# Performance work log

Hardware: AMD Instinct MI355X
Metric: run time of the kernel (lower is better)

The kernel has to match this reference:

```python
import jax, jax.numpy as jnp
import numpy as np

IN_F = 4096
OUT_F = 4096
GROUP = 128                      # quantization group size
NG = IN_F * OUT_F // GROUP       # 131072 groups
LORA_R = 16
LORA_SCALE = 32.0 / 16.0         # lora_alpha / lora_r


def _dequant(indices, codebook, scales):
    # Unpack two INT4 nibbles per byte: low nibble first, then high (interleaved).
    low = indices & 15
    high = (indices >> 4) & 15
    idx = jnp.stack([low, high], axis=1).reshape(-1)          # [numel]
    # Codebook lookup, per-group scaling.
    vals = codebook[idx].reshape(NG, GROUP) * scales[:, None]  # [NG, GROUP]
    return vals.reshape(OUT_F, IN_F)


def setup_inputs() -> dict:
    key = jax.random.key(0)
    ks = jax.random.split(key, 7)
    return {
        "x": jax.random.normal(ks[0], (4, 2048, IN_F), dtype=jnp.float32),
        "indices": jax.random.randint(ks[1], (IN_F * OUT_F // 2,), 0, 256, dtype=jnp.int32),
        "codebook": jax.random.normal(ks[2], (16,), dtype=jnp.float32),
        "scales": jax.random.uniform(ks[3], (NG,), dtype=jnp.float32, minval=0.01, maxval=1.0),
        "lora_A": jax.random.normal(ks[4], (IN_F, LORA_R), dtype=jnp.float32) / 64.0,
        "lora_B": jax.random.normal(ks[5], (LORA_R, OUT_F), dtype=jnp.float32) / 64.0,
        "bias": jax.random.normal(ks[6], (OUT_F,), dtype=jnp.float32),
    }


def reference(x, indices, codebook, scales, lora_A, lora_B, bias):
    # lowram path: dequantize INT4 codebook weights, F.linear, fused LoRA add, bias.
    W = _dequant(indices, codebook, scales)                    # [OUT_F, IN_F]
    h = jnp.einsum('bsi,oi->bso', x, W)                        # F.linear (no bias yet)
    h = h + (x @ lora_A) @ lora_B * LORA_SCALE                 # LoRA adapter (dropout=0)
    return h + bias
```

## Files before the change

kernel.cpp:

```cpp
#include <hip/hip_runtime.h>
#include <stdint.h>

#define IN_F   4096
#define OUT_F  4096
#define M_TOT  8192
#define KDIM   4096

typedef float          f32x4  __attribute__((ext_vector_type(4)));
typedef int            i32x4  __attribute__((ext_vector_type(4)));
typedef unsigned short u16x8  __attribute__((ext_vector_type(8)));
typedef __bf16         bf16x8 __attribute__((ext_vector_type(8)));

__device__ __forceinline__ unsigned short f2bf(float f) {
  uint32_t u = __builtin_bit_cast(uint32_t, f);
  u = (u + 0x7FFFu + ((u >> 16) & 1u)) >> 16;
  return (unsigned short)u;
}

__device__ __forceinline__ void gld_lds16(const void* g, void* l) {
  __builtin_amdgcn_global_load_lds((const __attribute__((address_space(1))) void*)g,
                                   (__attribute__((address_space(3))) void*)l,
                                   16, 0, 0);
}

__global__ __launch_bounds__(256) void k_xcast(const f32x4* __restrict__ x,
                                               u16x8* __restrict__ xb) {
  int t = blockIdx.x * 256 + threadIdx.x;
  f32x4 a = x[2 * t];
  f32x4 b = x[2 * t + 1];
  u16x8 o;
  o[0] = f2bf(a[0]); o[1] = f2bf(a[1]); o[2] = f2bf(a[2]); o[3] = f2bf(a[3]);
  o[4] = f2bf(b[0]); o[5] = f2bf(b[1]); o[6] = f2bf(b[2]); o[7] = f2bf(b[3]);
  xb[t] = o;
}

__global__ __launch_bounds__(256) void k_lora(const float* __restrict__ A,
                                              const float* __restrict__ Bm,
                                              float* __restrict__ L) {
  __shared__ float sB[16][64];
  const int ib = blockIdx.x * 256;
  const int ob = blockIdx.y * 64;
  const int t  = threadIdx.x;
  for (int j = 0; j < 4; ++j) {
    int idx = t + j * 256;
    int r = idx >> 6, oc = idx & 63;
    sB[r][oc] = Bm[r * OUT_F + ob + oc];
  }
  float a[16];
  const f32x4* Ap = (const f32x4*)(A + (size_t)(ib + t) * 16);
  #pragma unroll
  for (int j = 0; j < 4; ++j) {
    f32x4 v = Ap[j];
    a[4*j+0] = v[0]; a[4*j+1] = v[1]; a[4*j+2] = v[2]; a[4*j+3] = v[3];
  }
  __syncthreads();
  float* Lp = L + (size_t)ob * IN_F + ib + t;
  #pragma unroll 4
  for (int oc = 0; oc < 64; ++oc) {
    float acc = 0.f;
    #pragma unroll
    for (int r = 0; r < 16; ++r) acc += a[r] * sB[r][oc];
    Lp[(size_t)oc * IN_F] = acc * 2.0f;
  }
}

__global__ __launch_bounds__(256) void k_dequant(const int* __restrict__ idx,
                                                 const float* __restrict__ cb,
                                                 const float* __restrict__ scales,
                                                 const float* __restrict__ L,
                                                 unsigned short* __restrict__ Wc) {
  __shared__ float scb[16];
  const int t = blockIdx.x * 256 + threadIdx.x;
  if (threadIdx.x < 16) scb[threadIdx.x] = cb[threadIdx.x];
  __syncthreads();
  i32x4 w = ((const i32x4*)idx)[t];
  float sc = scales[t >> 4];
  f32x4 l0 = ((const f32x4*)L)[2 * t];
  f32x4 l1 = ((const f32x4*)L)[2 * t + 1];
  float lv[8] = {l0[0], l0[1], l0[2], l0[3], l1[0], l1[1], l1[2], l1[3]};
  u16x8 o;
  #pragma unroll
  for (int j = 0; j < 4; ++j) {
    int word = w[j];
    float v0 = scb[word & 15] * sc + lv[2 * j];
    float v1 = scb[(word >> 4) & 15] * sc + lv[2 * j + 1];
    o[2 * j]     = f2bf(v0);
    o[2 * j + 1] = f2bf(v1);
  }
  ((u16x8*)Wc)[t] = o;
}


#define BARR()  __builtin_amdgcn_s_barrier()
#define LGKM0() asm volatile("s_waitcnt lgkmcnt(0)" ::: "memory")
#define VMC6()  asm volatile("s_waitcnt vmcnt(6)" ::: "memory")
#define VMC0()  asm volatile("s_waitcnt vmcnt(0)" ::: "memory")

#define STAGE_A(kt, ha, c) do {                                                          \
  gld_lds16(Ag + (size_t)((ha) * 128) * KDIM + (kt) * 64,                                \
            smem + (c) * 32768 + (ha) * 16384 + ldsw);                                   \
  gld_lds16(Ag + (size_t)((ha) * 128 + 64) * KDIM + (kt) * 64,                           \
            smem + (c) * 32768 + (ha) * 16384 + 8192 + ldsw);                            \
} while (0)

#define STAGE_B(kt, hb, c) do {                                                          \
  gld_lds16(Bg + (size_t)((hb) * 128) * KDIM + (kt) * 64,                                \
            smem + 65536 + (c) * 32768 + (hb) * 16384 + ldsw);                           \
  gld_lds16(Bg + (size_t)((hb) * 128 + 64) * KDIM + (kt) * 64,                           \
            smem + 65536 + (c) * 32768 + (hb) * 16384 + 8192 + ldsw);                    \
} while (0)

#define LOAD_A(qm, c) do {                                                               \
  const char* _p = smem + (c) * 32768 + rowA + (qm) * 8192;                              \
  _Pragma("unroll")                                                                      \
  for (int mi = 0; mi < 4; ++mi) {                                                       \
    af[mi][0] = *(const bf16x8*)(_p + mi * 2048 + coff0);                                \
    af[mi][1] = *(const bf16x8*)(_p + mi * 2048 + coff1);                                \
  }                                                                                      \
} while (0)

#define LOAD_B(c) do {                                                                   \
  const char* _p = smem + 65536 + (c) * 32768 + rowB;                                    \
  _Pragma("unroll")                                                                      \
  for (int ni = 0; ni < 4; ++ni) {                                                       \
    bfr[ni][0] = *(const bf16x8*)(_p + ni * 2048 + coff0);                               \
    bfr[ni][1] = *(const bf16x8*)(_p + ni * 2048 + coff1);                               \
  }                                                                                      \
} while (0)

#define MFMA_PH(qm, nb) do {                                                             \
  __builtin_amdgcn_s_setprio(1);                                                         \
  _Pragma("unroll")                                                                      \
  for (int mi = 0; mi < 4; ++mi)                                                         \
    _Pragma("unroll")                                                                    \
    for (int nj = 0; nj < 2; ++nj)                                                       \
      _Pragma("unroll")                                                                  \
      for (int kk = 0; kk < 2; ++kk)                                                     \
        acc[(qm) * 4 + mi][(nb) * 2 + nj] = __builtin_amdgcn_mfma_f32_16x16x32_bf16(     \
            af[mi][kk], bfr[(nb) * 2 + nj][kk], acc[(qm) * 4 + mi][(nb) * 2 + nj],       \
            0, 0, 0);                                                                    \
  __builtin_amdgcn_s_setprio(0);                                                         \
} while (0)

#define TILE(t_, c_, doS4, doS123, VMCODE) do {                                          \
                                                                                \
  LOAD_A(0, c_); LOAD_B(c_);                                                             \
  if (doS4) STAGE_A((t_) + 1, 1, (c_) ^ 1);                                              \
  BARR(); LGKM0(); MFMA_PH(0, 0); BARR();                                                \
                                                                                \
  if (doS123) STAGE_B((t_) + 2, 0, c_);                                                  \
  BARR(); MFMA_PH(0, 1); BARR();                                                         \
                                                                                \
  LOAD_A(1, c_);                                                                         \
  if (doS123) STAGE_B((t_) + 2, 1, c_);                                                  \
  BARR(); LGKM0(); MFMA_PH(1, 1); BARR();                                                \
                                                                                \
  if (doS123) STAGE_A((t_) + 2, 0, c_);                                                  \
  BARR(); MFMA_PH(1, 0); VMCODE; BARR();                                                 \
} while (0)

__global__ __launch_bounds__(512, 2) void k_gemm(const unsigned short* __restrict__ A,
                                                 const unsigned short* __restrict__ B,
                                                 const float* __restrict__ bias,
                                                 float* __restrict__ C) {
  __shared__ char smem[131072];
  const int tid  = threadIdx.x;
  const int lane = tid & 63;
  const int wv   = tid >> 6;
  const int wm   = wv >> 2;
  const int wn   = wv & 3;
  const int r    = lane & 15;
  const int q    = lane >> 4;
  const int xr   = r & 7;
  const int coff0 = (q ^ xr) << 4;
  const int coff1 = ((q + 4) ^ xr) << 4;
  const int rowA = (wm * 128 + r) * 128;
  const int rowB = (wn * 64 + r) * 128;
  const int srow = tid >> 3;
  const int scol = ((tid & 7) ^ ((tid >> 3) & 7)) * 8;
  const int ldsw = wv * 1024;
  const int bm = blockIdx.x;
  const int bn = blockIdx.y;

  const unsigned short* Ag = A + (size_t)(bm * 256 + srow) * KDIM + scol;
  const unsigned short* Bg = B + (size_t)(bn * 256 + srow) * KDIM + scol;

  bf16x8 af[4][2], bfr[4][2];
  f32x4 acc[8][4];
  #pragma unroll
  for (int m = 0; m < 8; ++m)
    #pragma unroll
    for (int n = 0; n < 4; ++n)
      acc[m][n] = (f32x4){0.f, 0.f, 0.f, 0.f};

  STAGE_B(0, 0, 0); STAGE_B(0, 1, 0); STAGE_A(0, 0, 0); STAGE_A(0, 1, 0);
  STAGE_B(1, 0, 1); STAGE_B(1, 1, 1); STAGE_A(1, 0, 1);
  VMC6();
  BARR();

  #pragma unroll 1
  for (int t = 0; t < 62; t += 2) {
    TILE(t,     0, 1, 1, VMC6());
    TILE(t + 1, 1, 1, 1, VMC6());
  }
  TILE(62, 0, 1, 0, VMC0());
  TILE(63, 1, 0, 0, VMC0());

  const int row0 = bm * 256 + wm * 128;
  const int col0 = bn * 256 + wn * 64;
  float bv[4];
  #pragma unroll
  for (int ni = 0; ni < 4; ++ni) bv[ni] = bias[col0 + ni * 16 + r];
  #pragma unroll
  for (int mi = 0; mi < 8; ++mi) {
    #pragma unroll
    for (int j = 0; j < 4; ++j) {
      const int row = row0 + mi * 16 + q * 4 + j;
      float* Cp = C + (size_t)row * OUT_F + col0 + r;
      #pragma unroll
      for (int ni = 0; ni < 4; ++ni)
        Cp[ni * 16] = acc[mi][ni][j] + bv[ni];
    }
  }
}

extern "C" void kernel_launch(void* const* d_in, const int* in_sizes, int n_in,
                              void* d_out, int out_size, void* d_ws, size_t ws_size,
                              hipStream_t stream) {
  const float* x    = (const float*)d_in[0];
  const int*   idx  = (const int*)d_in[1];
  const float* cb   = (const float*)d_in[2];
  const float* scl  = (const float*)d_in[3];
  const float* lA   = (const float*)d_in[4];
  const float* lB   = (const float*)d_in[5];
  const float* bias = (const float*)d_in[6];
  float* out = (float*)d_out;

  unsigned short* xb = (unsigned short*)d_ws;
  unsigned short* Wc = (unsigned short*)((char*)d_ws + (size_t)M_TOT * KDIM * 2);
  float* Lbuf = out;

  k_xcast<<<16384, 256, 0, stream>>>((const f32x4*)x, (u16x8*)xb);
  k_lora<<<dim3(16, 64), 256, 0, stream>>>(lA, lB, Lbuf);
  k_dequant<<<8192, 256, 0, stream>>>(idx, cb, scl, Lbuf, Wc);
  k_gemm<<<dim3(32, 16), 512, 0, stream>>>(xb, Wc, bias, out);
}
```

Baseline: 289.8 us.

## Store LoRA delta as bf16, split B fragment loads, remap blocks across XCDs

Three separate changes. The LoRA delta buffer is written and read as bf16 instead of fp32, which halves that intermediate's traffic at the cost of an extra rounding before the add. In the GEMM, B-fragment LDS reads are split into two halves interleaved with the MFMA phases, and global-to-LDS staging is reordered to cut register pressure and shift load timing. A 1D grid with a swizzled block id spreads neighbouring tiles across the eight XCDs, aiming for better L2 reuse.

```diff
diff --git a/kernel.cpp b/kernel.cpp
--- a/kernel.cpp
+++ b/kernel.cpp
@@ -15,6 +15,9 @@
   uint32_t u = __builtin_bit_cast(uint32_t, f);
   u = (u + 0x7FFFu + ((u >> 16) & 1u)) >> 16;
   return (unsigned short)u;
+}
+__device__ __forceinline__ float bf2f(unsigned short s) {
+  return __builtin_bit_cast(float, (uint32_t)s << 16);
 }
 
 __device__ __forceinline__ void gld_lds16(const void* g, void* l) {
@@ -36,7 +39,7 @@
 
 __global__ __launch_bounds__(256) void k_lora(const float* __restrict__ A,
                                               const float* __restrict__ Bm,
-                                              float* __restrict__ L) {
+                                              unsigned short* __restrict__ L) {
   __shared__ float sB[16][64];
   const int ib = blockIdx.x * 256;
   const int ob = blockIdx.y * 64;
@@ -54,20 +57,20 @@
     a[4*j+0] = v[0]; a[4*j+1] = v[1]; a[4*j+2] = v[2]; a[4*j+3] = v[3];
   }
   __syncthreads();
-  float* Lp = L + (size_t)ob * IN_F + ib + t;
+  unsigned short* Lp = L + (size_t)ob * IN_F + ib + t;
   #pragma unroll 4
   for (int oc = 0; oc < 64; ++oc) {
     float acc = 0.f;
     #pragma unroll
     for (int r = 0; r < 16; ++r) acc += a[r] * sB[r][oc];
-    Lp[(size_t)oc * IN_F] = acc * 2.0f;
+    Lp[(size_t)oc * IN_F] = f2bf(acc * 2.0f);
   }
 }
 
 __global__ __launch_bounds__(256) void k_dequant(const int* __restrict__ idx,
                                                  const float* __restrict__ cb,
                                                  const float* __restrict__ scales,
-                                                 const float* __restrict__ L,
+                                                 const unsigned short* __restrict__ L,
                                                  unsigned short* __restrict__ Wc) {
   __shared__ float scb[16];
   const int t = blockIdx.x * 256 + threadIdx.x;
@@ -75,15 +78,13 @@
   __syncthreads();
   i32x4 w = ((const i32x4*)idx)[t];
   float sc = scales[t >> 4];
-  f32x4 l0 = ((const f32x4*)L)[2 * t];
-  f32x4 l1 = ((const f32x4*)L)[2 * t + 1];
-  float lv[8] = {l0[0], l0[1], l0[2], l0[3], l1[0], l1[1], l1[2], l1[3]};
+  u16x8 lw = ((const u16x8*)L)[t];
   u16x8 o;
   #pragma unroll
   for (int j = 0; j < 4; ++j) {
     int word = w[j];
-    float v0 = scb[word & 15] * sc + lv[2 * j];
-    float v1 = scb[(word >> 4) & 15] * sc + lv[2 * j + 1];
+    float v0 = scb[word & 15] * sc + bf2f(lw[2 * j]);
+    float v1 = scb[(word >> 4) & 15] * sc + bf2f(lw[2 * j + 1]);
     o[2 * j]     = f2bf(v0);
     o[2 * j + 1] = f2bf(v1);
   }
@@ -119,10 +120,19 @@
   }                                                                                      \
 } while (0)
 
-#define LOAD_B(c) do {                                                                   \
+#define LOAD_B01(c) do {                                                                 \
   const char* _p = smem + 65536 + (c) * 32768 + rowB;                                    \
   _Pragma("unroll")                                                                      \
-  for (int ni = 0; ni < 4; ++ni) {                                                       \
+  for (int ni = 0; ni < 2; ++ni) {                                                       \
+    bfr[ni][0] = *(const bf16x8*)(_p + ni * 2048 + coff0);                               \
+    bfr[ni][1] = *(const bf16x8*)(_p + ni * 2048 + coff1);                               \
+  }                                                                                      \
+} while (0)
+
+#define LOAD_B23(c) do {                                                                 \
+  const char* _p = smem + 65536 + (c) * 32768 + rowB;                                    \
+  _Pragma("unroll")                                                                      \
+  for (int ni = 2; ni < 4; ++ni) {                                                       \
     bfr[ni][0] = *(const bf16x8*)(_p + ni * 2048 + coff0);                               \
     bfr[ni][1] = *(const bf16x8*)(_p + ni * 2048 + coff1);                               \
   }                                                                                      \
@@ -144,18 +154,18 @@
 
 #define TILE(t_, c_, doS4, doS123, VMCODE) do {                                          \
                                                                                 \
-  LOAD_A(0, c_); LOAD_B(c_);                                                             \
+  LOAD_A(0, c_); LOAD_B01(c_);                                                           \
   if (doS4) STAGE_A((t_) + 1, 1, (c_) ^ 1);                                              \
   BARR(); LGKM0(); MFMA_PH(0, 0); BARR();                                                \
                                                                                 \
+  LOAD_B23(c_);                                                                          \
+  BARR(); LGKM0(); MFMA_PH(0, 1); BARR();                                                \
+                                                                                \
+  LOAD_A(1, c_);                                                                         \
   if (doS123) STAGE_B((t_) + 2, 0, c_);                                                  \
-  BARR(); MFMA_PH(0, 1); BARR();                                                         \
-                                                                                \
-  LOAD_A(1, c_);                                                                         \
-  if (doS123) STAGE_B((t_) + 2, 1, c_);                                                  \
   BARR(); LGKM0(); MFMA_PH(1, 1); BARR();                                                \
                                                                                 \
-  if (doS123) STAGE_A((t_) + 2, 0, c_);                                                  \
+  if (doS123) { STAGE_B((t_) + 2, 1, c_); STAGE_A((t_) + 2, 0, c_); }                    \
   BARR(); MFMA_PH(1, 0); VMCODE; BARR();                                                 \
 } while (0)
 
@@ -179,8 +189,11 @@
   const int srow = tid >> 3;
   const int scol = ((tid & 7) ^ ((tid >> 3) & 7)) * 8;
   const int ldsw = wv * 1024;
-  const int bm = blockIdx.x;
-  const int bn = blockIdx.y;
+
+  const int id  = blockIdx.x;
+  const int sid = ((id & 7) << 6) | (id >> 3);
+  const int bm  = sid & 31;
+  const int bn  = sid >> 5;
 
   const unsigned short* Ag = A + (size_t)(bm * 256 + srow) * KDIM + scol;
   const unsigned short* Bg = B + (size_t)(bn * 256 + srow) * KDIM + scol;
@@ -238,10 +251,10 @@
 
   unsigned short* xb = (unsigned short*)d_ws;
   unsigned short* Wc = (unsigned short*)((char*)d_ws + (size_t)M_TOT * KDIM * 2);
-  float* Lbuf = out;
+  unsigned short* Lbuf = (unsigned short*)d_out;
 
   k_xcast<<<16384, 256, 0, stream>>>((const f32x4*)x, (u16x8*)xb);
   k_lora<<<dim3(16, 64), 256, 0, stream>>>(lA, lB, Lbuf);
   k_dequant<<<8192, 256, 0, stream>>>(idx, cb, scl, Lbuf, Wc);
-  k_gemm<<<dim3(32, 16), 512, 0, stream>>>(xb, Wc, bias, out);
-}
+  k_gemm<<<512, 512, 0, stream>>>(xb, Wc, bias, out);
+}
```

Measured after the change: 299.7 us. +3.4%, slower.
